# Kernel optimization log

Hardware: AMD Instinct MI355X
Metric: run time of the kernel (lower is better)

## Reference

```python
import jax, jax.numpy as jnp
import numpy as np

COMPRESSION = 2  # max-pool factor along flattened spatial axis for phi and g


def setup_inputs() -> dict:
    key = jax.random.key(0)
    ks = jax.random.split(key, 5)
    B, C, H, W = 4, 64, 96, 96
    Ci = 32  # intermediate_dim = C // 2
    s = 1.0 / np.sqrt(C)
    return {
        "x": jax.random.normal(ks[0], (B, C, H, W), dtype=jnp.float32),
        "w_theta": jax.random.normal(ks[1], (Ci, C), dtype=jnp.float32) * s,
        "b_theta": jnp.zeros((Ci,), dtype=jnp.float32),
        "w_phi": jax.random.normal(ks[2], (Ci, C), dtype=jnp.float32) * s,
        "b_phi": jnp.zeros((Ci,), dtype=jnp.float32),
        "w_g": jax.random.normal(ks[3], (Ci, C), dtype=jnp.float32) * s,
        "b_g": jnp.zeros((Ci,), dtype=jnp.float32),
        "w_out": jax.random.normal(ks[4], (C, Ci), dtype=jnp.float32) * (1.0 / np.sqrt(Ci)),
        "b_out": jnp.zeros((C,), dtype=jnp.float32),
    }


def reference(x, w_theta, b_theta, w_phi, b_phi, w_g, b_g, w_out, b_out):
    B, C, H, W = x.shape
    N = H * W
    xf = x.reshape(B, C, N).transpose(0, 2, 1)            # [B, N, C]
    # 1x1 conv projections == channel matmuls
    theta = xf @ w_theta.T + b_theta                      # [B, N, Ci]
    phi = xf @ w_phi.T + b_phi                            # [B, N, Ci]
    g = xf @ w_g.T + b_g                                  # [B, N, Ci]
    # compression: max-pool (kernel=stride=COMPRESSION) along flattened spatial axis
    Ci = theta.shape[-1]
    phi = phi.reshape(B, N // COMPRESSION, COMPRESSION, Ci).max(axis=2)  # [B, N/c, Ci]
    g = g.reshape(B, N // COMPRESSION, COMPRESSION, Ci).max(axis=2)      # [B, N/c, Ci]
    # embedded-gaussian affinity + softmax
    attn = jax.nn.softmax(jnp.einsum('bnc,bmc->bnm', theta, phi), axis=-1)  # [B, N, N/c]
    y = jnp.einsum('bnm,bmc->bnc', attn, g)               # [B, N, Ci]
    out = y @ w_out.T + b_out                             # [B, N, C]
    out = out.transpose(0, 2, 1).reshape(B, C, H, W)
    return out + x  # residual
```

## Files before the change

kernel.cpp:

```cpp
#include <hip/hip_runtime.h>
#include <hip/hip_bf16.h>


#define NQ 9216
#define MM 4608
#define TPW 36
#define LOG2E 1.44269504088896340736f

typedef __attribute__((ext_vector_type(8))) short bf16x8;
typedef __attribute__((ext_vector_type(4))) float f32x4;
typedef __attribute__((ext_vector_type(4))) unsigned short u16x4;

static __device__ __forceinline__ unsigned pk2(float a, float b) {
    __hip_bfloat162 h = __float22bfloat162_rn(make_float2(a, b));
    return *reinterpret_cast<unsigned*>(&h);
}

__global__ __launch_bounds__(128, 4) void proj_kernel(
    const float* __restrict__ x,
    const float* __restrict__ wt, const float* __restrict__ bt,
    const float* __restrict__ wp, const float* __restrict__ bp,
    const float* __restrict__ wg, const float* __restrict__ bg,
    unsigned short* __restrict__ theta, unsigned short* __restrict__ phi,
    unsigned short* __restrict__ gT)
{
    __shared__ unsigned short gst[32 * 20];

    const int tid  = threadIdx.x;
    const int wid  = tid >> 6;
    const int lane = tid & 63;
    const int q = lane >> 4;
    const int c = lane & 15;

    const int b     = blockIdx.x / 288;
    const int rem   = blockIdx.x % 288;
    const int n0    = rem * 32 + wid * 16;

    const float* Wm[3] = {wt, wp, wg};
    const float* Bm[3] = {bt, bp, bg};

    bf16x8 wf[3][2][2];
    float bias[3][2];
#pragma unroll
    for (int p = 0; p < 3; ++p) {
#pragma unroll
        for (int ct = 0; ct < 2; ++ct) {
            bias[p][ct] = Bm[p][ct * 16 + c];
#pragma unroll
            for (int ks = 0; ks < 2; ++ks) {
                const float* wsrc = Wm[p] + (ct * 16 + c) * 64 + ks * 32 + q * 8;
                f32x4 w0 = *(const f32x4*)wsrc;
                f32x4 w1 = *(const f32x4*)(wsrc + 4);
                unsigned* wk = (unsigned*)&wf[p][ct][ks];
                wk[0] = pk2(w0[0], w0[1]); wk[1] = pk2(w0[2], w0[3]);
                wk[2] = pk2(w1[0], w1[1]); wk[3] = pk2(w1[2], w1[3]);
            }
        }
    }

    bf16x8 af[2];
#pragma unroll
    for (int ks = 0; ks < 2; ++ks) {
        unsigned* ap = (unsigned*)&af[ks];
#pragma unroll
        for (int j2 = 0; j2 < 4; ++j2) {
            float x0 = x[(b * 64 + ks * 32 + q * 8 + j2 * 2) * NQ + n0 + c];
            float x1 = x[(b * 64 + ks * 32 + q * 8 + j2 * 2 + 1) * NQ + n0 + c];
            ap[j2] = pk2(x0, x1);
        }
    }

#pragma unroll
    for (int p = 0; p < 3; ++p) {
#pragma unroll
        for (int ct = 0; ct < 2; ++ct) {
            f32x4 acc = {0.f, 0.f, 0.f, 0.f};
            acc = __builtin_amdgcn_mfma_f32_16x16x32_bf16(af[0], wf[p][ct][0], acc, 0, 0, 0);
            acc = __builtin_amdgcn_mfma_f32_16x16x32_bf16(af[1], wf[p][ct][1], acc, 0, 0, 0);
#pragma unroll
            for (int r = 0; r < 4; ++r) acc[r] += bias[p][ct];
            const int ci = ct * 16 + c;
            if (p == 0) {
                unsigned pv0 = pk2(acc[0] * LOG2E, acc[1] * LOG2E);
                unsigned pv1 = pk2(acc[2] * LOG2E, acc[3] * LOG2E);
                theta[(b * NQ + n0 + 4 * q + 0) * 32 + ci] = (unsigned short)pv0;
                theta[(b * NQ + n0 + 4 * q + 1) * 32 + ci] = (unsigned short)(pv0 >> 16);
                theta[(b * NQ + n0 + 4 * q + 2) * 32 + ci] = (unsigned short)pv1;
                theta[(b * NQ + n0 + 4 * q + 3) * 32 + ci] = (unsigned short)(pv1 >> 16);
            } else {
                unsigned pv = pk2(fmaxf(acc[0], acc[1]), fmaxf(acc[2], acc[3]));
                if (p == 1) {
                    const int m0 = (n0 >> 1) + 2 * q;
                    phi[(b * MM + m0) * 32 + ci]     = (unsigned short)pv;
                    phi[(b * MM + m0 + 1) * 32 + ci] = (unsigned short)(pv >> 16);
                } else {
                    *(unsigned int*)(gst + ci * 20 + wid * 8 + 2 * q) = pv;
                }
            }
        }
    }

    __syncthreads();
    {
        const int ci = tid >> 2;
        const int m4 = (tid & 3) * 4;
        u16x4 v = *(const u16x4*)(gst + ci * 20 + m4);
        *(u16x4*)(gT + (b * 32 + ci) * MM + rem * 16 + m4) = v;
    }
}

__global__ __launch_bounds__(256, 5) void attn_kernel(
    const unsigned short* __restrict__ theta, const unsigned short* __restrict__ phi,
    const unsigned short* __restrict__ gT,
    const float* __restrict__ w_out, const float* __restrict__ b_out,
    const float* __restrict__ x, float* __restrict__ out)
{
    __shared__ unsigned short pld[4][32 * 32];
    __shared__ float red[4][32][36];
    __shared__ float lred[4][32];
    __shared__ unsigned short yld[32 * 34];

    const int tid  = threadIdx.x;
    const int w    = tid >> 6;
    const int lane = tid & 63;
    const int q  = lane >> 4;
    const int c  = lane & 15;
    const int sw = ((c >> 1) & 3) << 3;

    const int b  = blockIdx.x / 288;
    const int nb = (blockIdx.x % 288) * 32;

    bf16x8 qf[2];
#pragma unroll
    for (int rt = 0; rt < 2; ++rt)
        qf[rt] = *(const bf16x8*)(theta + (b * NQ + nb + rt * 16 + c) * 32 + q * 8);

    bf16x8 onef;
    {
        unsigned v = (c == 0) ? 0x3F803F80u : 0u;
        unsigned* op = (unsigned*)&onef;
        op[0] = v; op[1] = v; op[2] = v; op[3] = v;
    }

    const unsigned short* phiB = phi + (size_t)b * MM * 32;
    const unsigned short* gTB  = gT + (size_t)b * 32 * MM;
    unsigned short* myp = pld[w];

    f32x4 acc[2][2];
    f32x4 lacc[2];
#pragma unroll
    for (int rt = 0; rt < 2; ++rt) {
        lacc[rt] = (f32x4){0.f, 0.f, 0.f, 0.f};
#pragma unroll
        for (int s2 = 0; s2 < 2; ++s2) acc[rt][s2] = (f32x4){0.f, 0.f, 0.f, 0.f};
    }

    const int t0 = w * TPW;
    bf16x8 kf[2], vf[2];

#define LOAD_KF(m0) do {                                                      \
    kf[0] = *(const bf16x8*)(phiB + ((m0) + c) * 32 + q * 8);                 \
    kf[1] = *(const bf16x8*)(phiB + ((m0) + 16 + c) * 32 + q * 8);            \
} while (0)

#define LOAD_VF(m0) do {                                                      \
    vf[0] = *(const bf16x8*)(gTB + c * MM + (m0) + q * 8);                    \
    vf[1] = *(const bf16x8*)(gTB + (16 + c) * MM + (m0) + q * 8);             \
} while (0)

#define S_STEP(rt) do {                                                      \
    _Pragma("unroll")                                                        \
    for (int mct = 0; mct < 2; ++mct) {                                      \
        f32x4 z = {0.f, 0.f, 0.f, 0.f};                                      \
        f32x4 s = __builtin_amdgcn_mfma_f32_16x16x32_bf16(kf[mct], qf[rt], z, 0, 0, 0); \
        uint2 hv = {pk2(__builtin_amdgcn_exp2f(s[0]), __builtin_amdgcn_exp2f(s[1])),    \
                    pk2(__builtin_amdgcn_exp2f(s[2]), __builtin_amdgcn_exp2f(s[3]))};   \
        *(uint2*)(myp + (((rt) * 16 + c) << 5) + ((mct * 16 + 4 * q) ^ sw)) = hv;       \
    }                                                                        \
} while (0)

#define PV_STEP(rt) do {                                                     \
    bf16x8 pf = *(const bf16x8*)(myp + (((rt) * 16 + c) << 5) + ((q * 8) ^ sw)); \
    acc[rt][0] = __builtin_amdgcn_mfma_f32_16x16x32_bf16(vf[0], pf, acc[rt][0], 0, 0, 0); \
    acc[rt][1] = __builtin_amdgcn_mfma_f32_16x16x32_bf16(vf[1], pf, acc[rt][1], 0, 0, 0); \
    lacc[rt]   = __builtin_amdgcn_mfma_f32_16x16x32_bf16(onef,  pf, lacc[rt],   0, 0, 0); \
} while (0)

    LOAD_KF(t0 * 32);
    LOAD_VF(t0 * 32);
    S_STEP(0); S_STEP(1);

    for (int mi = 1; mi < TPW; ++mi) {
        const int m0 = (t0 + mi) * 32;
        LOAD_KF(m0);
        PV_STEP(0); PV_STEP(1);
        LOAD_VF(m0);
        S_STEP(0); S_STEP(1);
    }

    PV_STEP(0); PV_STEP(1);

#undef LOAD_KF
#undef LOAD_VF
#undef S_STEP
#undef PV_STEP

    if (lane < 16) {
        lred[w][lane]      = lacc[0][0];
        lred[w][16 + lane] = lacc[1][0];
    }
#pragma unroll
    for (int rt = 0; rt < 2; ++rt)
#pragma unroll
        for (int s2 = 0; s2 < 2; ++s2)
            *(f32x4*)&red[w][rt * 16 + c][s2 * 16 + 4 * q] = acc[rt][s2];

    __syncthreads();

    {
        const int n  = tid & 31;
        const int cg = (tid >> 5) * 4;
        float ls = (lred[0][n] + lred[1][n]) + (lred[2][n] + lred[3][n]);
        float inv = 1.0f / ls;
        f32x4 s = {0.f, 0.f, 0.f, 0.f};
#pragma unroll
        for (int ww = 0; ww < 4; ++ww)
            s += *(const f32x4*)&red[ww][n][cg];
#pragma unroll
        for (int k = 0; k < 4; ++k)
            yld[(cg + k) * 34 + n] = (unsigned short)(pk2(s[k] * inv, 0.f) & 0xffff);
    }
    __syncthreads();

    {
        bf16x8 wof;
        {
            const float* wsrc = w_out + (w * 16 + c) * 32 + q * 8;
            f32x4 w0 = *(const f32x4*)wsrc;
            f32x4 w1 = *(const f32x4*)(wsrc + 4);
            unsigned* wk = (unsigned*)&wof;
            wk[0] = pk2(w0[0], w0[1]); wk[1] = pk2(w0[2], w0[3]);
            wk[2] = pk2(w1[0], w1[1]); wk[3] = pk2(w1[2], w1[3]);
        }
#pragma unroll
        for (int nt = 0; nt < 2; ++nt) {
            bf16x8 yf;
            unsigned short* yp = (unsigned short*)&yf;
#pragma unroll
            for (int j = 0; j < 8; ++j)
                yp[j] = yld[(q * 8 + j) * 34 + nt * 16 + c];
            f32x4 z = {0.f, 0.f, 0.f, 0.f};
            f32x4 o = __builtin_amdgcn_mfma_f32_16x16x32_bf16(wof, yf, z, 0, 0, 0);
#pragma unroll
            for (int r = 0; r < 4; ++r) {
                const int chn = w * 16 + 4 * q + r;
                const size_t addr = (size_t)(b * 64 + chn) * NQ + nb + nt * 16 + c;
                out[addr] = o[r] + b_out[chn] + x[addr];
            }
        }
    }
}

extern "C" void kernel_launch(void* const* d_in, const int* in_sizes, int n_in,
                              void* d_out, int out_size, void* d_ws, size_t ws_size,
                              hipStream_t stream) {
    const float* x       = (const float*)d_in[0];
    const float* w_theta = (const float*)d_in[1];
    const float* b_theta = (const float*)d_in[2];
    const float* w_phi   = (const float*)d_in[3];
    const float* b_phi   = (const float*)d_in[4];
    const float* w_g     = (const float*)d_in[5];
    const float* b_g     = (const float*)d_in[6];
    const float* w_out   = (const float*)d_in[7];
    const float* b_out   = (const float*)d_in[8];
    float* out = (float*)d_out;

    unsigned short* theta = (unsigned short*)d_ws;
    unsigned short* phi   = theta + 4 * NQ * 32;
    unsigned short* gT    = phi + 4 * MM * 32;

    proj_kernel<<<1152, 128, 0, stream>>>(x, w_theta, b_theta, w_phi, b_phi,
                                          w_g, b_g, theta, phi, gT);
    attn_kernel<<<1152, 256, 0, stream>>>(theta, phi, gT, w_out, b_out, x, out);
}
```

Before: 147.5 us.

## Widen attention tile to 48 queries over 6 waves with double-buffered K/V loads

Each attention block now handles 48 query rows instead of 32 and splits the keys across 6 waves, each covering 24 key tiles. This raises reuse of every loaded phi/g fragment from two to three query subtiles. K/V fragments are double-buffered so the next tile's loads are issued before the current MFMA work. The P tile buffer and the reduction buffers now share LDS through a union, which requires an extra barrier, and only four of the six waves run the output projection.

Result: slower. 172.0 us (+16.6%).

```diff
diff --git a/kernel.cpp b/kernel.cpp
--- a/kernel.cpp
+++ b/kernel.cpp
@@ -4,7 +4,7 @@
 
 #define NQ 9216
 #define MM 4608
-#define TPW 36
+#define TPW 24
 #define LOG2E 1.44269504088896340736f
 
 typedef __attribute__((ext_vector_type(8))) short bf16x8;
@@ -109,16 +109,20 @@
     }
 }
 
-__global__ __launch_bounds__(256, 5) void attn_kernel(
+__global__ __launch_bounds__(384, 5) void attn_kernel(
     const unsigned short* __restrict__ theta, const unsigned short* __restrict__ phi,
     const unsigned short* __restrict__ gT,
     const float* __restrict__ w_out, const float* __restrict__ b_out,
     const float* __restrict__ x, float* __restrict__ out)
 {
-    __shared__ unsigned short pld[4][32 * 32];
-    __shared__ float red[4][32][36];
-    __shared__ float lred[4][32];
-    __shared__ unsigned short yld[32 * 34];
+    __shared__ union SharedU {
+        unsigned short pld[6][48 * 32];
+        struct {
+            float red[6][48][36];
+            float lred[6][48];
+            unsigned short yld[32][50];
+        } ep;
+    } sh;
 
     const int tid  = threadIdx.x;
     const int w    = tid >> 6;
@@ -127,12 +131,12 @@
     const int c  = lane & 15;
     const int sw = ((c >> 1) & 3) << 3;
 
-    const int b  = blockIdx.x / 288;
-    const int nb = (blockIdx.x % 288) * 32;
-
-    bf16x8 qf[2];
-#pragma unroll
-    for (int rt = 0; rt < 2; ++rt)
+    const int b  = blockIdx.x / 192;
+    const int nb = (blockIdx.x % 192) * 48;
+
+    bf16x8 qf[3];
+#pragma unroll
+    for (int rt = 0; rt < 3; ++rt)
         qf[rt] = *(const bf16x8*)(theta + (b * NQ + nb + rt * 16 + c) * 32 + q * 8);
 
     bf16x8 onef;
@@ -144,95 +148,107 @@
 
     const unsigned short* phiB = phi + (size_t)b * MM * 32;
     const unsigned short* gTB  = gT + (size_t)b * 32 * MM;
-    unsigned short* myp = pld[w];
-
-    f32x4 acc[2][2];
-    f32x4 lacc[2];
-#pragma unroll
-    for (int rt = 0; rt < 2; ++rt) {
+    unsigned short* myp = sh.pld[w];
+
+    f32x4 acc[3][2];
+    f32x4 lacc[3];
+#pragma unroll
+    for (int rt = 0; rt < 3; ++rt) {
         lacc[rt] = (f32x4){0.f, 0.f, 0.f, 0.f};
 #pragma unroll
         for (int s2 = 0; s2 < 2; ++s2) acc[rt][s2] = (f32x4){0.f, 0.f, 0.f, 0.f};
     }
 
     const int t0 = w * TPW;
-    bf16x8 kf[2], vf[2];
-
-#define LOAD_KF(m0) do {                                                      \
-    kf[0] = *(const bf16x8*)(phiB + ((m0) + c) * 32 + q * 8);                 \
-    kf[1] = *(const bf16x8*)(phiB + ((m0) + 16 + c) * 32 + q * 8);            \
-} while (0)
-
-#define LOAD_VF(m0) do {                                                      \
-    vf[0] = *(const bf16x8*)(gTB + c * MM + (m0) + q * 8);                    \
-    vf[1] = *(const bf16x8*)(gTB + (16 + c) * MM + (m0) + q * 8);             \
-} while (0)
-
-#define S_STEP(rt) do {                                                      \
+    bf16x8 kfA[2], kfB[2], vfA[2], vfB[2];
+
+#define LOAD_KF(DST, m0) do {                                                 \
+    DST[0] = *(const bf16x8*)(phiB + ((m0) + c) * 32 + q * 8);                \
+    DST[1] = *(const bf16x8*)(phiB + ((m0) + 16 + c) * 32 + q * 8);           \
+} while (0)
+
+#define LOAD_VF(DST, m0) do {                                                 \
+    DST[0] = *(const bf16x8*)(gTB + c * MM + (m0) + q * 8);                   \
+    DST[1] = *(const bf16x8*)(gTB + (16 + c) * MM + (m0) + q * 8);            \
+} while (0)
+
+#define S_STEP(rt, KF) do {                                                  \
     _Pragma("unroll")                                                        \
     for (int mct = 0; mct < 2; ++mct) {                                      \
         f32x4 z = {0.f, 0.f, 0.f, 0.f};                                      \
-        f32x4 s = __builtin_amdgcn_mfma_f32_16x16x32_bf16(kf[mct], qf[rt], z, 0, 0, 0); \
+        f32x4 s = __builtin_amdgcn_mfma_f32_16x16x32_bf16(KF[mct], qf[rt], z, 0, 0, 0); \
         uint2 hv = {pk2(__builtin_amdgcn_exp2f(s[0]), __builtin_amdgcn_exp2f(s[1])),    \
                     pk2(__builtin_amdgcn_exp2f(s[2]), __builtin_amdgcn_exp2f(s[3]))};   \
         *(uint2*)(myp + (((rt) * 16 + c) << 5) + ((mct * 16 + 4 * q) ^ sw)) = hv;       \
     }                                                                        \
 } while (0)
 
-#define PV_STEP(rt) do {                                                     \
+#define PV_STEP(rt, VF) do {                                                 \
     bf16x8 pf = *(const bf16x8*)(myp + (((rt) * 16 + c) << 5) + ((q * 8) ^ sw)); \
-    acc[rt][0] = __builtin_amdgcn_mfma_f32_16x16x32_bf16(vf[0], pf, acc[rt][0], 0, 0, 0); \
-    acc[rt][1] = __builtin_amdgcn_mfma_f32_16x16x32_bf16(vf[1], pf, acc[rt][1], 0, 0, 0); \
+    acc[rt][0] = __builtin_amdgcn_mfma_f32_16x16x32_bf16(VF[0], pf, acc[rt][0], 0, 0, 0); \
+    acc[rt][1] = __builtin_amdgcn_mfma_f32_16x16x32_bf16(VF[1], pf, acc[rt][1], 0, 0, 0); \
     lacc[rt]   = __builtin_amdgcn_mfma_f32_16x16x32_bf16(onef,  pf, lacc[rt],   0, 0, 0); \
 } while (0)
 
-    LOAD_KF(t0 * 32);
-    LOAD_VF(t0 * 32);
-    S_STEP(0); S_STEP(1);
-
-    for (int mi = 1; mi < TPW; ++mi) {
-        const int m0 = (t0 + mi) * 32;
-        LOAD_KF(m0);
-        PV_STEP(0); PV_STEP(1);
-        LOAD_VF(m0);
-        S_STEP(0); S_STEP(1);
-    }
-
-    PV_STEP(0); PV_STEP(1);
+#define ITER(mi, KC, KN, VC, VN, DO_KN) do {                                 \
+    if (DO_KN) LOAD_KF(KN, (t0 + (mi) + 1) * 32);                            \
+    LOAD_VF(VN, (t0 + (mi)) * 32);                                           \
+    PV_STEP(0, VC); PV_STEP(1, VC); PV_STEP(2, VC);                          \
+    S_STEP(0, KC); S_STEP(1, KC); S_STEP(2, KC);                             \
+} while (0)
+
+    LOAD_KF(kfB, t0 * 32);
+    LOAD_VF(vfA, t0 * 32);
+    LOAD_KF(kfA, (t0 + 1) * 32);
+    S_STEP(0, kfB); S_STEP(1, kfB); S_STEP(2, kfB);
+
+    for (int mi = 1; mi + 1 < TPW; mi += 2) {
+        ITER(mi,     kfA, kfB, vfA, vfB, 1);
+        ITER(mi + 1, kfB, kfA, vfB, vfA, 1);
+    }
+    ITER(TPW - 1, kfA, kfB, vfA, vfB, 0);
+
+    PV_STEP(0, vfB); PV_STEP(1, vfB); PV_STEP(2, vfB);
 
 #undef LOAD_KF
 #undef LOAD_VF
 #undef S_STEP
 #undef PV_STEP
+#undef ITER
+
+    __syncthreads();
 
     if (lane < 16) {
-        lred[w][lane]      = lacc[0][0];
-        lred[w][16 + lane] = lacc[1][0];
-    }
-#pragma unroll
-    for (int rt = 0; rt < 2; ++rt)
+        sh.ep.lred[w][lane]      = lacc[0][0];
+        sh.ep.lred[w][16 + lane] = lacc[1][0];
+        sh.ep.lred[w][32 + lane] = lacc[2][0];
+    }
+#pragma unroll
+    for (int rt = 0; rt < 3; ++rt)
 #pragma unroll
         for (int s2 = 0; s2 < 2; ++s2)
-            *(f32x4*)&red[w][rt * 16 + c][s2 * 16 + 4 * q] = acc[rt][s2];
+            *(f32x4*)&sh.ep.red[w][rt * 16 + c][s2 * 16 + 4 * q] = acc[rt][s2];
 
     __syncthreads();
 
     {
-        const int n  = tid & 31;
-        const int cg = (tid >> 5) * 4;
-        float ls = (lred[0][n] + lred[1][n]) + (lred[2][n] + lred[3][n]);
+        const int n  = tid % 48;
+        const int cg = (tid / 48) * 4;
+        float ls = ((sh.ep.lred[0][n] + sh.ep.lred[1][n]) +
+                    (sh.ep.lred[2][n] + sh.ep.lred[3][n])) +
+                   (sh.ep.lred[4][n] + sh.ep.lred[5][n]);
         float inv = 1.0f / ls;
         f32x4 s = {0.f, 0.f, 0.f, 0.f};
 #pragma unroll
-        for (int ww = 0; ww < 4; ++ww)
-            s += *(const f32x4*)&red[ww][n][cg];
+        for (int ww = 0; ww < 6; ++ww)
+            s += *(const f32x4*)&sh.ep.red[ww][n][cg];
 #pragma unroll
         for (int k = 0; k < 4; ++k)
-            yld[(cg + k) * 34 + n] = (unsigned short)(pk2(s[k] * inv, 0.f) & 0xffff);
+            sh.ep.yld[cg + k][n] = (unsigned short)(pk2(s[k] * inv, 0.f) & 0xffff);
     }
     __syncthreads();
 
-    {
+    if (w < 4) {
         bf16x8 wof;
         {
             const float* wsrc = w_out + (w * 16 + c) * 32 + q * 8;
@@ -243,12 +259,12 @@
             wk[2] = pk2(w1[0], w1[1]); wk[3] = pk2(w1[2], w1[3]);
         }
 #pragma unroll
-        for (int nt = 0; nt < 2; ++nt) {
+        for (int nt = 0; nt < 3; ++nt) {
             bf16x8 yf;
             unsigned short* yp = (unsigned short*)&yf;
 #pragma unroll
             for (int j = 0; j < 8; ++j)
-                yp[j] = yld[(q * 8 + j) * 34 + nt * 16 + c];
+                yp[j] = sh.ep.yld[q * 8 + j][nt * 16 + c];
             f32x4 z = {0.f, 0.f, 0.f, 0.f};
             f32x4 o = __builtin_amdgcn_mfma_f32_16x16x32_bf16(wof, yf, z, 0, 0, 0);
 #pragma unroll
@@ -281,5 +297,5 @@
 
     proj_kernel<<<1152, 128, 0, stream>>>(x, w_theta, b_theta, w_phi, b_phi,
                                           w_g, b_g, theta, phi, gT);
-    attn_kernel<<<1152, 256, 0, stream>>>(theta, phi, gT, w_out, b_out, x, out);
+    attn_kernel<<<768, 384, 0, stream>>>(theta, phi, gT, w_out, b_out, x, out);
 }
```
